# Performance work log

Measured on AMD Instinct MI355X. Metric: run time of the kernel, lower is better.

Reference implementation:

```python
import jax, jax.numpy as jnp
import numpy as np

# node types: 0=atac_region 1=gene 2=tad 3=protein 4=protein_name 5=enhancer
N = [25000, 15000, 4000, 12000, 12000, 15000]
FEAT = [257, 129, 128, 128, 129, 128]
# 19 relations of the HeteroConv, as (src_type, dst_type)
REL = [(2,0),(0,2),(2,1),(1,2),(0,1),(1,0),(3,3),(3,1),(1,3),(3,1),(1,3),(3,4),(4,3),(5,0),(0,5),(5,1),(1,5),(0,1),(1,0)]
E = 100000
H, HID = 128, 256
NAMES = ['atac','gene','tad','protein','pname','enh']


def setup_inputs():
    rng = np.random.default_rng(0)
    w = lambda *s: jnp.asarray((rng.standard_normal(s) / np.sqrt(s[-2])).astype(np.float32))
    z = lambda *s: jnp.zeros(s, dtype=jnp.float32)
    inp = {}
    for L in (0, 1):
        for t, nm in enumerate(NAMES):
            inp[f"x_{nm}{L}"] = jnp.asarray(rng.standard_normal((N[t], FEAT[t])).astype(np.float32))
            # sorted unique global node ids (x_map)
            inp[f"map_{nm}{L}"] = jnp.asarray(np.sort(rng.choice(2 * N[t], size=N[t], replace=False)).astype(np.int32))
        e = np.empty((len(REL), 2, E), dtype=np.int32)
        for r, (s, d) in enumerate(REL):
            e[r, 0] = rng.integers(0, N[s], E)
            e[r, 1] = rng.integers(0, N[d], E)
        inp[f"edges{L}"] = jnp.asarray(e)
    inp.update(W_in_atac=w(257, H), b_in_atac=z(H), W_in_gene=w(129, H), b_in_gene=z(H), W_in_pname=w(129, H), b_in_pname=z(H))
    inp.update(conv_wl=w(19, H, H), conv_bl=z(19, H), conv_wr=w(19, H, H))
    inp.update(mlp_w1=w(6, H, HID), mlp_b1=z(6, HID), mlp_w2=w(6, HID, H), mlp_b2=z(6, H))
    inp.update(gd_w1=w(H, HID), gd_b1=z(HID), gd_w2=w(HID, 1), gd_b2=z(1),
               gv_w1=w(H, HID), gv_b1=z(HID), gv_w2=w(HID, 1), gv_b2=z(1))
    return inp


def _sage(x_src, x_dst, eidx, wl, bl, wr):
    # PyG SAGEConv: out = lin_l(mean_{j in N(i)} x_src[j]) + lin_r(x_dst[i])
    src, dst = eidx[0], eidx[1]
    nd = x_dst.shape[0]
    agg = jax.ops.segment_sum(x_src[src], dst, num_segments=nd)
    cnt = jax.ops.segment_sum(jnp.ones((src.shape[0],), x_src.dtype), dst, num_segments=nd)
    mean = agg / jnp.maximum(cnt, 1.0)[:, None]
    return mean @ wl + bl + x_dst @ wr


def _hetero(xs, edges, wl, bl, wr):
    # HeteroConv with default sum aggregation across relations sharing a dst type
    out = {}
    for r, (s, d) in enumerate(REL):
        o = _sage(xs[s], xs[d], edges[r], wl[r], bl[r], wr[r])
        out[d] = out[d] + o if d in out else o
    return out


def _forward(fl, maps0, maps1, edges0, edges1):
    (x_atac0, x_gene0, x_tad0, x_protein0, x_pname0, x_enh0,
     x_atac1, x_gene1, x_tad1, x_protein1, x_pname1, x_enh1,
     W_in_atac, b_in_atac, W_in_gene, b_in_gene, W_in_pname, b_in_pname,
     conv_wl, conv_bl, conv_wr,
     mlp_w1, mlp_b1, mlp_w2, mlp_b2,
     gd_w1, gd_b1, gd_w2, gd_b2, gv_w1, gv_b1, gv_w2, gv_b2) = fl
    # input_linear applied to protein_name / atac_region / gene of every layer snapshot
    xs0 = [x_atac0 @ W_in_atac + b_in_atac, x_gene0 @ W_in_gene + b_in_gene, x_tad0,
           x_protein0, x_pname0 @ W_in_pname + b_in_pname, x_enh0]
    xs1 = [x_atac1 @ W_in_atac + b_in_atac, x_gene1 @ W_in_gene + b_in_gene, x_tad1,
           x_protein1, x_pname1 @ W_in_pname + b_in_pname, x_enh1]
    # layer 0 hetero conv + per-node-type layer MLP
    new0 = _hetero(xs0, edges0, conv_wl, conv_bl, conv_wr)
    new0 = {d: jax.nn.relu(x @ mlp_w1[d] + mlp_b1[d]) @ mlp_w2[d] + mlp_b2[d] for d, x in new0.items()}
    # mask-based cross-layer scatter: next_layer.x[dst_mask] = new_x[src_mask]
    # (x_maps sorted & unique -> equivalent gather via argmax of the O(N^2) equality mask)
    for d, x in new0.items():
        Mm = maps0[d][:, None] == maps1[d][None, :]   # [N0_d, N1_d] bool
        dst_mask = Mm.any(axis=0)                      # next-layer nodes present in layer 0
        pos = jnp.argmax(Mm, axis=0)                   # matching layer-0 row per next node
        xs1[d] = jnp.where(dst_mask[:, None], x[pos], xs1[d])
    # final layer: hetero conv only (no layer MLP, per encode())
    new1 = _hetero(xs1, edges1, conv_wl, conv_bl, conv_wr)
    g = new1[1]  # target = 'gene'
    p_drop = jax.nn.sigmoid(jax.nn.relu(g @ gd_w1 + gd_b1) @ gd_w2 + gd_b2)
    values = jax.nn.relu(g @ gv_w1 + gv_b1) @ gv_w2 + gv_b2
    return jnp.concatenate([p_drop, values], axis=-1)  # [N_gene, 2]


def reference(x_atac0, x_gene0, x_tad0, x_protein0, x_pname0, x_enh0,
              x_atac1, x_gene1, x_tad1, x_protein1, x_pname1, x_enh1,
              map_atac0, map_gene0, map_tad0, map_protein0, map_pname0, map_enh0,
              map_atac1, map_gene1, map_tad1, map_protein1, map_pname1, map_enh1,
              edges0, edges1,
              W_in_atac, b_in_atac, W_in_gene, b_in_gene, W_in_pname, b_in_pname,
              conv_wl, conv_bl, conv_wr,
              mlp_w1, mlp_b1, mlp_w2, mlp_b2,
              gd_w1, gd_b1, gd_w2, gd_b2, gv_w1, gv_b1, gv_w2, gv_b2):
    maps0 = [map_atac0, map_gene0, map_tad0, map_protein0, map_pname0, map_enh0]
    maps1 = [map_atac1, map_gene1, map_tad1, map_protein1, map_pname1, map_enh1]
    fl = (x_atac0, x_gene0, x_tad0, x_protein0, x_pname0, x_enh0,
          x_atac1, x_gene1, x_tad1, x_protein1, x_pname1, x_enh1,
          W_in_atac, b_in_atac, W_in_gene, b_in_gene, W_in_pname, b_in_pname,
          conv_wl, conv_bl, conv_wr,
          mlp_w1, mlp_b1, mlp_w2, mlp_b2,
          gd_w1, gd_b1, gd_w2, gd_b2, gv_w1, gv_b1, gv_w2, gv_b2)
    return _forward(fl, maps0, maps1, edges0, edges1)
```

## Files before the change

### kernel.cpp

```cpp
#include <hip/hip_runtime.h>
#include <math.h>

#define E_EDGES 100000

typedef unsigned short u16;
typedef unsigned int u32;

using bfrag = __attribute__((ext_vector_type(8))) short;
using ffrag = __attribute__((ext_vector_type(4))) float;

__device__ inline float bf2f(u32 u) { union { u32 i; float f; } c; c.i = u << 16; return c.f; }
__device__ inline u16 f2bf(float f) {
  union { u32 i; float f; } c; c.f = f;
  u32 u = c.i;
  return (u16)((u + 0x7FFFu + ((u >> 16) & 1u)) >> 16);
}

struct CsrArgs { int relid[24]; int lay[24]; int nd[24]; int rpoff[24];
                 int bkoff[24]; int bboff[24]; int nb[24]; };

struct AggAllArgs {
  const u16* xsrc[18];
  const int* rowptr[18];
  const int* esrc[18];
  u16* dst[18];
  int nd[18]; int pitch[18]; int koff[18];
};

struct WTStackArgs {
  int srcrel[23]; int grp[23]; long outoff[23]; int koff[23]; int pitch[23];
  int gnr[5]; int grel[5][6];
};

struct WTArgs { const float* W[15]; u16* out[15]; int K[15]; int N[15]; int Kpad[15]; };
struct PadArgs { const float* src[11]; u16* dst[11]; int K[11]; int Kpad8[11];
                 int total[11]; int aligned[11]; };
struct InLinBArgs { const u16* A[5]; const u16* WT[5]; const float* bias[5]; u16* C[5];
                    int M[5]; int Kpad[5]; };
struct FusedArgs {
  const u16* A[5]; const u16* selfA[5]; const u16* WTC[5]; const float* biasC[5];
  const u16* W1[5]; const float* b1[5]; const u16* W2[5]; const float* b2[5];
  const int* POS[5]; u16* C[5]; int M[5]; int kself[5]; int Kpad[5];
};
struct PosArgs { const int* m0[5]; const int* m1[5]; int* pos[5]; int n[5]; };
struct HeadArgs { const u16* WT[2]; const float* b1[2]; float* hid[2]; const u16* A; int M; };
struct HeadRArgs { const float* hid[2]; const float* w2[2]; const float* b2[2]; float* out; int M; };

__global__ __launch_bounds__(256) void tgemm_inb(InLinBArgs a)
{
  const int z = blockIdx.z;
  const int M = a.M[z], Kpad = a.Kpad[z];
  const int rowbase = blockIdx.x * 64;
  if (rowbase >= M) return;
  __shared__ u16 sA[64 * 40];
  __shared__ u16 sB[128 * 40];
  const int tid = threadIdx.x;
  const int w = tid >> 6, lane = tid & 63;
  const int quad = lane >> 4, m = lane & 15;
  const int sr = tid >> 2, sc = tid & 3;
  const int br = tid >> 1, bh = tid & 1;
  const u16* A = a.A[z];
  const u16* WT = a.WT[z];
  ffrag acc[8];
  #pragma unroll
  for (int i = 0; i < 8; i++) { acc[i][0] = 0.f; acc[i][1] = 0.f; acc[i][2] = 0.f; acc[i][3] = 0.f; }

  for (int kt = 0; kt < Kpad / 32; kt++) {
    int gr = rowbase + sr, gk = kt * 32 + sc * 8;
    uint4 st = make_uint4(0, 0, 0, 0);
    if (gr < M) st = *(const uint4*)(A + (long)gr * Kpad + gk);
    const u16* wrow = WT + (long)br * Kpad + kt * 32 + bh * 16;
    uint4 b0 = *(const uint4*)wrow;
    uint4 b1 = *(const uint4*)(wrow + 8);

    if (kt) __syncthreads();
    *(uint4*)&sA[sr * 40 + sc * 8] = st;
    *(uint4*)&sB[br * 40 + bh * 16] = b0;
    *(uint4*)&sB[br * 40 + bh * 16 + 8] = b1;
    __syncthreads();

    bfrag av = *(const bfrag*)&sA[(w * 16 + m) * 40 + quad * 8];
    #pragma unroll
    for (int ct = 0; ct < 8; ct++) {
      bfrag bv = *(const bfrag*)&sB[(ct * 16 + m) * 40 + quad * 8];
      acc[ct] = __builtin_amdgcn_mfma_f32_16x16x32_bf16(av, bv, acc[ct], 0, 0, 0);
    }
  }

  const float* bias = a.bias[z];
  u16* C = a.C[z];
  #pragma unroll
  for (int ct = 0; ct < 8; ct++) {
    int col = ct * 16 + m;
    float bv = bias[col];
    #pragma unroll
    for (int r = 0; r < 4; r++) {
      int row = rowbase + w * 16 + quad * 4 + r;
      if (row < M) C[(long)row * 128 + col] = f2bf(acc[ct][r] + bv);
    }
  }
}

__global__ __launch_bounds__(256) void fused_mlp(FusedArgs a)
{
  const int z = blockIdx.z;
  const int M = a.M[z];
  const int rowbase = blockIdx.x * 64;
  if (rowbase >= M) return;
  __shared__ u16 LDS[25088];
  u16* sB  = LDS;
  u16* sA  = LDS + 5120;
  u16* m1  = LDS + 7680;
  u16* m2b = LDS + 5120;
  u16* m2a = LDS + 16384;
  const int tid = threadIdx.x;
  const int w = tid >> 6, lane = tid & 63;
  const int quad = lane >> 4, m = lane & 15;
  const int sr = tid >> 2, sc = tid & 3;
  const int br = tid >> 1, bh = tid & 1;
  const int kself = a.kself[z], Kpad = a.Kpad[z];
  const u16* A = a.A[z];
  const u16* selfA = a.selfA[z];

  {
    const u16* WT = a.WTC[z];
    ffrag acc[8];
    #pragma unroll
    for (int i = 0; i < 8; i++) { acc[i][0] = 0.f; acc[i][1] = 0.f; acc[i][2] = 0.f; acc[i][3] = 0.f; }
    for (int kt = 0; kt < Kpad / 32; kt++) {
      int gr = rowbase + sr, gk = kt * 32 + sc * 8;
      uint4 st = make_uint4(0, 0, 0, 0);
      if (gr < M) {
        const u16* src = (gk < kself) ? (A + (long)gr * kself + gk)
                                      : (selfA + (long)gr * 128 + (gk - kself));
        st = *(const uint4*)src;
      }
      const u16* wrow = WT + (long)br * Kpad + kt * 32 + bh * 16;
      uint4 b0 = *(const uint4*)wrow;
      uint4 b1 = *(const uint4*)(wrow + 8);

      if (kt) __syncthreads();
      *(uint4*)&sA[sr * 40 + sc * 8] = st;
      *(uint4*)&sB[br * 40 + bh * 16] = b0;
      *(uint4*)&sB[br * 40 + bh * 16 + 8] = b1;
      __syncthreads();

      bfrag av = *(const bfrag*)&sA[(w * 16 + m) * 40 + quad * 8];
      #pragma unroll
      for (int ct = 0; ct < 8; ct++) {
        bfrag bv = *(const bfrag*)&sB[(ct * 16 + m) * 40 + quad * 8];
        acc[ct] = __builtin_amdgcn_mfma_f32_16x16x32_bf16(av, bv, acc[ct], 0, 0, 0);
      }
    }
    const float* bc = a.biasC[z];
    #pragma unroll
    for (int ct = 0; ct < 8; ct++) {
      int col = ct * 16 + m;
      float bv = bc[col];
      #pragma unroll
      for (int r = 0; r < 4; r++) {
        int row = w * 16 + quad * 4 + r;
        m1[row * 136 + col] = f2bf(acc[ct][r] + bv);
      }
    }
  }

  {
    const u16* W1 = a.W1[z];
    const float* b1p = a.b1[z];
    for (int h = 0; h < 2; h++) {
      ffrag acch[8];
      #pragma unroll
      for (int i = 0; i < 8; i++) { acch[i][0] = 0.f; acch[i][1] = 0.f; acch[i][2] = 0.f; acch[i][3] = 0.f; }
      for (int kt = 0; kt < 4; kt++) {
        const u16* wrow = W1 + (long)(h * 128 + br) * 128 + kt * 32 + bh * 16;
        uint4 b0 = *(const uint4*)wrow;
        uint4 b1v = *(const uint4*)(wrow + 8);
        __syncthreads();
        *(uint4*)&sB[br * 40 + bh * 16] = b0;
        *(uint4*)&sB[br * 40 + bh * 16 + 8] = b1v;
        __syncthreads();
        bfrag av = *(const bfrag*)&m1[(w * 16 + m) * 136 + kt * 32 + quad * 8];
        #pragma unroll
        for (int ct = 0; ct < 8; ct++) {
          bfrag bv = *(const bfrag*)&sB[(ct * 16 + m) * 40 + quad * 8];
          acch[ct] = __builtin_amdgcn_mfma_f32_16x16x32_bf16(av, bv, acch[ct], 0, 0, 0);
        }
      }
      u16* dstm = h ? m2b : m2a;
      if (h) __syncthreads();
      #pragma unroll
      for (int ct = 0; ct < 8; ct++) {
        int col = ct * 16 + m;
        float bv = b1p[h * 128 + col];
        #pragma unroll
        for (int r = 0; r < 4; r++) {
          int row = w * 16 + quad * 4 + r;
          dstm[row * 136 + col] = f2bf(fmaxf(acch[ct][r] + bv, 0.f));
        }
      }
    }
  }

  {
    const u16* W2 = a.W2[z];
    ffrag acc2[8];
    #pragma unroll
    for (int i = 0; i < 8; i++) { acc2[i][0] = 0.f; acc2[i][1] = 0.f; acc2[i][2] = 0.f; acc2[i][3] = 0.f; }
    for (int kt = 0; kt < 8; kt++) {
      const u16* wrow = W2 + (long)br * 256 + kt * 32 + bh * 16;
      uint4 b0 = *(const uint4*)wrow;
      uint4 b1v = *(const uint4*)(wrow + 8);
      __syncthreads();
      *(uint4*)&sB[br * 40 + bh * 16] = b0;
      *(uint4*)&sB[br * 40 + bh * 16 + 8] = b1v;
      __syncthreads();
      const u16* msrc = (kt < 4) ? m2a : m2b;
      bfrag av = *(const bfrag*)&msrc[(w * 16 + m) * 136 + (kt & 3) * 32 + quad * 8];
      #pragma unroll
      for (int ct = 0; ct < 8; ct++) {
        bfrag bv = *(const bfrag*)&sB[(ct * 16 + m) * 40 + quad * 8];
        acc2[ct] = __builtin_amdgcn_mfma_f32_16x16x32_bf16(av, bv, acc2[ct], 0, 0, 0);
      }
    }
    const int* POS = a.POS[z];
    const float* b2p = a.b2[z];
    u16* C = a.C[z];
    #pragma unroll
    for (int ct = 0; ct < 8; ct++) {
      int col = ct * 16 + m;
      float bv = b2p[col];
      #pragma unroll
      for (int r = 0; r < 4; r++) {
        int row = rowbase + w * 16 + quad * 4 + r;
        if (row < M) {
          int j = POS[row];
          if (j >= 0) C[(long)j * 128 + col] = f2bf(acc2[ct][r] + bv);
        }
      }
    }
  }
}

__global__ __launch_bounds__(256) void conv_l1(const u16* __restrict__ A,
                                               const u16* __restrict__ selfA,
                                               const u16* __restrict__ WT,
                                               const float* __restrict__ bias,
                                               u16* __restrict__ C,
                                               int M, int kself, int Kpad)
{
  const int rowbase = blockIdx.x * 64;
  if (rowbase >= M) return;
  __shared__ u16 sA[64 * 40];
  __shared__ u16 sB[128 * 40];
  const int tid = threadIdx.x;
  const int w = tid >> 6, lane = tid & 63;
  const int quad = lane >> 4, m = lane & 15;
  const int sr = tid >> 2, sc = tid & 3;
  const int br = tid >> 1, bh = tid & 1;
  ffrag acc[8];
  #pragma unroll
  for (int i = 0; i < 8; i++) { acc[i][0] = 0.f; acc[i][1] = 0.f; acc[i][2] = 0.f; acc[i][3] = 0.f; }

  for (int kt = 0; kt < Kpad / 32; kt++) {
    int gr = rowbase + sr, gk = kt * 32 + sc * 8;
    uint4 st = make_uint4(0, 0, 0, 0);
    if (gr < M) {
      const u16* src = (gk < kself) ? (A + (long)gr * kself + gk)
                                    : (selfA + (long)gr * 128 + (gk - kself));
      st = *(const uint4*)src;
    }
    const u16* wrow = WT + (long)br * Kpad + kt * 32 + bh * 16;
    uint4 b0 = *(const uint4*)wrow;
    uint4 b1 = *(const uint4*)(wrow + 8);

    if (kt) __syncthreads();
    *(uint4*)&sA[sr * 40 + sc * 8] = st;
    *(uint4*)&sB[br * 40 + bh * 16] = b0;
    *(uint4*)&sB[br * 40 + bh * 16 + 8] = b1;
    __syncthreads();

    bfrag av = *(const bfrag*)&sA[(w * 16 + m) * 40 + quad * 8];
    #pragma unroll
    for (int ct = 0; ct < 8; ct++) {
      bfrag bv = *(const bfrag*)&sB[(ct * 16 + m) * 40 + quad * 8];
      acc[ct] = __builtin_amdgcn_mfma_f32_16x16x32_bf16(av, bv, acc[ct], 0, 0, 0);
    }
  }

  #pragma unroll
  for (int ct = 0; ct < 8; ct++) {
    int col = ct * 16 + m;
    float bv = bias[col];
    #pragma unroll
    for (int r = 0; r < 4; r++) {
      int row = rowbase + w * 16 + quad * 4 + r;
      if (row < M) C[(long)row * 128 + col] = f2bf(acc[ct][r] + bv);
    }
  }
}

__global__ __launch_bounds__(256) void padcvt_kernel(PadArgs a)
{
  const int z = blockIdx.y;
  int idx = blockIdx.x * 256 + threadIdx.x;
  if (idx >= a.total[z]) return;
  const int kp8 = a.Kpad8[z];
  const int K = a.K[z];
  int row = idx / kp8;
  int c8 = idx - row * kp8;
  int base = c8 * 8;
  u32 wv[4];
  if (a.aligned[z]) {
    const float4* src = (const float4*)(a.src[z] + (long)row * K + base);
    float4 f0 = src[0];
    float4 f1 = src[1];
    wv[0] = (u32)f2bf(f0.x) | ((u32)f2bf(f0.y) << 16);
    wv[1] = (u32)f2bf(f0.z) | ((u32)f2bf(f0.w) << 16);
    wv[2] = (u32)f2bf(f1.x) | ((u32)f2bf(f1.y) << 16);
    wv[3] = (u32)f2bf(f1.z) | ((u32)f2bf(f1.w) << 16);
  } else {
    const float* src = a.src[z] + (long)row * K + base;
    #pragma unroll
    for (int i = 0; i < 4; i++) {
      float lo = (base + 2 * i     < K) ? src[2 * i]     : 0.f;
      float hi = (base + 2 * i + 1 < K) ? src[2 * i + 1] : 0.f;
      wv[i] = (u32)f2bf(lo) | ((u32)f2bf(hi) << 16);
    }
  }
  *(uint4*)(a.dst[z] + (long)row * (kp8 * 8) + base) = make_uint4(wv[0], wv[1], wv[2], wv[3]);
}

__global__ __launch_bounds__(256) void tgemm_head(HeadArgs a)
{
  const int z = blockIdx.z;
  const int M = a.M;
  const int rowbase = blockIdx.x * 64;
  const int colbase = blockIdx.y * 128;
  __shared__ u16 sA[64 * 40];
  __shared__ u16 sB[128 * 40];
  const int tid = threadIdx.x;
  const int w = tid >> 6, lane = tid & 63;
  const int quad = lane >> 4, m = lane & 15;
  const int sr = tid >> 2, sc = tid & 3;
  const int br = tid >> 1, bh = tid & 1;
  const u16* A = a.A;
  const u16* WT = a.WT[z];
  ffrag acc[8];
  #pragma unroll
  for (int i = 0; i < 8; i++) { acc[i][0] = 0.f; acc[i][1] = 0.f; acc[i][2] = 0.f; acc[i][3] = 0.f; }

  for (int kt = 0; kt < 4; kt++) {
    int gr = rowbase + sr, gk = kt * 32 + sc * 8;
    uint4 st = make_uint4(0, 0, 0, 0);
    if (gr < M) st = *(const uint4*)(A + (long)gr * 128 + gk);
    const u16* wrow = WT + (long)(colbase + br) * 128 + kt * 32 + bh * 16;
    uint4 b0 = *(const uint4*)wrow;
    uint4 b1 = *(const uint4*)(wrow + 8);

    if (kt) __syncthreads();
    *(uint4*)&sA[sr * 40 + sc * 8] = st;
    *(uint4*)&sB[br * 40 + bh * 16] = b0;
    *(uint4*)&sB[br * 40 + bh * 16 + 8] = b1;
    __syncthreads();

    bfrag av = *(const bfrag*)&sA[(w * 16 + m) * 40 + quad * 8];
    #pragma unroll
    for (int ct = 0; ct < 8; ct++) {
      bfrag bv = *(const bfrag*)&sB[(ct * 16 + m) * 40 + quad * 8];
      acc[ct] = __builtin_amdgcn_mfma_f32_16x16x32_bf16(av, bv, acc[ct], 0, 0, 0);
    }
  }

  const float* bias = a.b1[z];
  float* C = a.hid[z];
  #pragma unroll
  for (int ct = 0; ct < 8; ct++) {
    int col = colbase + ct * 16 + m;
    float bv = bias[col];
    #pragma unroll
    for (int r = 0; r < 4; r++) {
      int row = rowbase + w * 16 + quad * 4 + r;
      if (row < M) C[(long)row * 256 + col] = fmaxf(acc[ct][r] + bv, 0.f);
    }
  }
}

__global__ __launch_bounds__(256) void bhist_kernel(const int* __restrict__ e0,
                                                    const int* __restrict__ e1,
                                                    int* __restrict__ bcnt, CsrArgs a)
{
  const int slot = blockIdx.x / 25;
  const int ch = blockIdx.x % 25;
  const int base = ch * 4096;
  const int n = (E_EDGES - base < 4096) ? (E_EDGES - base) : 4096;
  const int* E = a.lay[slot] ? e1 : e0;
  const int r = a.relid[slot];
  const int tid = threadIdx.x;
  __shared__ int h[256];
  h[tid] = 0;
  __syncthreads();
  const int* darr = E + (r * 2 + 1) * E_EDGES + base;
  for (int i = tid; i < n; i += 256) atomicAdd(&h[darr[i] >> 7], 1);
  __syncthreads();
  if (tid < a.nb[slot] && h[tid]) atomicAdd(&bcnt[a.bkoff[slot] + tid], h[tid]);
}

__global__ __launch_bounds__(256) void bscan_kernel(const int* __restrict__ bcnt,
                                                    int* __restrict__ bbase,
                                                    int* __restrict__ bcur, CsrArgs a)
{
  int slot = blockIdx.x;
  int nb = a.nb[slot];
  int tid = threadIdx.x, lane = tid & 63, w = tid >> 6;
  __shared__ int ws[4];
  int v = (tid < nb) ? bcnt[a.bkoff[slot] + tid] : 0;
  int si = v;
  #pragma unroll
  for (int off = 1; off < 64; off <<= 1) {
    int t = __shfl_up(si, off, 64);
    if (lane >= off) si += t;
  }
  if (lane == 63) ws[w] = si;
  __syncthreads();
  int woff = 0;
  #pragma unroll
  for (int k = 0; k < 4; k++) if (k < w) woff += ws[k];
  int excl = woff + si - v;
  if (tid < nb) { bbase[a.bboff[slot] + tid] = excl; bcur[a.bkoff[slot] + tid] = excl; }
  if (tid == 0) bbase[a.bboff[slot] + nb] = ws[0] + ws[1] + ws[2] + ws[3];
}

__global__ __launch_bounds__(256) void bucket_scatter(const int* __restrict__ e0,
                                                      const int* __restrict__ e1,
                                                      int* __restrict__ bcur,
                                                      u32* __restrict__ tmp, CsrArgs a)
{
  const int slot = blockIdx.x / 25;
  const int ch = blockIdx.x % 25;
  const int base = ch * 4096;
  const int n = (E_EDGES - base < 4096) ? (E_EDGES - base) : 4096;
  const int* E = a.lay[slot] ? e1 : e0;
  const int r = a.relid[slot];
  const int nb = a.nb[slot];
  const int tid = threadIdx.x;
  __shared__ int hist[256], start[256], gbase[256], lcur[256];
  __shared__ u32 sorted[4096];
  hist[tid] = 0;
  __syncthreads();
  const int* darr = E + (r * 2 + 1) * E_EDGES + base;
  const int* sarr = E + r * 2 * E_EDGES + base;
  for (int i = tid; i < n; i += 256) atomicAdd(&hist[darr[i] >> 7], 1);
  __syncthreads();
  if (tid == 0) {
    int s = 0;
    for (int b = 0; b < nb; b++) { start[b] = s; s += hist[b]; }
  }
  __syncthreads();
  if (tid < nb) {
    gbase[tid] = atomicAdd(&bcur[a.bkoff[slot] + tid], hist[tid]);
    lcur[tid] = start[tid];
  }
  __syncthreads();
  for (int i = tid; i < n; i += 256) {
    int dst = darr[i], src = sarr[i];
    int pos = atomicAdd(&lcur[dst >> 7], 1);
    sorted[pos] = ((u32)dst << 16) | (u32)src;
  }
  __syncthreads();
  u32* out = tmp + (long)slot * E_EDGES;
  for (int i = tid; i < n; i += 256) {
    u32 p = sorted[i];
    int b = p >> 23;
    out[gbase[b] + (i - start[b])] = p;
  }
}

__global__ __launch_bounds__(256) void bucket_to_csr(const u32* __restrict__ tmp,
                                                     const int* __restrict__ bbase,
                                                     int* __restrict__ rp,
                                                     int* __restrict__ esrc, CsrArgs a)
{
  const int b = blockIdx.x, slot = blockIdx.y;
  if (b >= a.nb[slot]) return;
  const int rb = a.rpoff[slot];
  const int bb = bbase[a.bboff[slot] + b];
  const int be = bbase[a.bboff[slot] + b + 1];
  const int cnt = be - bb;
  const int rowlo = b << 7;
  int rowhi = rowlo + 128; if (rowhi > a.nd[slot]) rowhi = a.nd[slot];
  const int nrow = rowhi - rowlo;
  const int tid = threadIdx.x;
  __shared__ int rcnt[128];
  __shared__ int rpref[129];
  __shared__ int scur[128];
  __shared__ u32 sbuf[8192];
  if (tid < 128) rcnt[tid] = 0;
  __syncthreads();
  const u32* in = tmp + (long)slot * E_EDGES + bb;
  for (int i = tid; i < cnt; i += 256) atomicAdd(&rcnt[(in[i] >> 16) & 127], 1);
  __syncthreads();
  if (tid == 0) {
    int s = 0;
    for (int t = 0; t < 128; t++) { rpref[t] = s; s += rcnt[t]; }
    rpref[128] = s;
  }
  __syncthreads();
  if (tid < nrow) rp[rb + rowlo + tid] = bb + rpref[tid];
  if (tid == 0) rp[rb + rowhi] = be;
  if (tid < 128) scur[tid] = rpref[tid];
  __syncthreads();
  int* out = esrc + (long)slot * E_EDGES + bb;
  if (cnt <= 8192) {
    for (int i = tid; i < cnt; i += 256) {
      u32 p = in[i];
      int pos = atomicAdd(&scur[(p >> 16) & 127], 1);
      sbuf[pos] = p & 0xFFFFu;
    }
    __syncthreads();
    for (int i = tid; i < cnt; i += 256) out[i] = (int)sbuf[i];
  } else {
    for (int i = tid; i < cnt; i += 256) {
      u32 p = in[i];
      int pos = atomicAdd(&scur[(p >> 16) & 127], 1);
      out[pos] = (int)(p & 0xFFFFu);
    }
  }
}

__global__ __launch_bounds__(256) void wtstack_kernel(const float* __restrict__ wl,
                                                      const float* __restrict__ wr,
                                                      const float* __restrict__ bl,
                                                      u16* __restrict__ WTG,
                                                      float* __restrict__ BLS, WTStackArgs a)
{
  int slot = blockIdx.y;
  int t = blockIdx.x * 256 + threadIdx.x;
  int krel = t & 127, n = t >> 7;
  int sr = a.srcrel[slot];
  float v;
  if (sr >= 0) {
    v = wl[(long)sr * 16384 + krel * 128 + n];
  } else {
    int g = a.grp[slot];
    v = 0.f;
    for (int i = 0; i < a.gnr[g]; i++) v += wr[(long)a.grel[g][i] * 16384 + krel * 128 + n];
    if (t < 128) {
      float b = 0.f;
      for (int i = 0; i < a.gnr[g]; i++) b += bl[a.grel[g][i] * 128 + t];
      BLS[g * 128 + t] = b;
    }
  }
  WTG[a.outoff[slot] + (long)n * a.pitch[slot] + a.koff[slot] + krel] = f2bf(v);
}

__global__ __launch_bounds__(256) void wt_kernel(WTArgs a)
{
  int s = blockIdx.y;
  int idx = blockIdx.x * 256 + threadIdx.x;
  int K = a.K[s], N = a.N[s], Kpad = a.Kpad[s];
  if (idx >= N * Kpad) return;
  int n = idx / Kpad, k = idx - n * Kpad;
  a.out[s][idx] = (k < K) ? f2bf(a.W[s][(long)k * N + n]) : (u16)0;
}

__global__ __launch_bounds__(256) void pos_kernel(PosArgs a)
{
  int g = blockIdx.y;
  int i = blockIdx.x * 256 + threadIdx.x;
  if (i >= a.n[g]) return;
  int key = a.m0[g][i];
  const int* m1 = a.m1[g];
  int lo = 0, hi = a.n[g] - 1, pos = -1;
  while (lo <= hi) {
    int mid = (lo + hi) >> 1;
    int v = m1[mid];
    if (v == key) { pos = mid; break; }
    if (v < key) lo = mid + 1; else hi = mid - 1;
  }
  a.pos[g][i] = pos;
}

__global__ __launch_bounds__(256) void agg_all(AggAllArgs a)
{
  int slot = blockIdx.y;
  int grp = threadIdx.x >> 4;
  int lane = threadIdx.x & 15;
  int row = blockIdx.x * 16 + grp;
  if (row >= a.nd[slot]) return;
  u16* dst = a.dst[slot] + (long)row * a.pitch[slot] + a.koff[slot] + lane * 8;
  const uint4* x4 = (const uint4*)a.xsrc[slot];
  const int* rp = a.rowptr[slot];
  int c0 = rp[row], c1 = rp[row + 1];
  const int* es = a.esrc[slot];
  float acc[8];
  #pragma unroll
  for (int i = 0; i < 8; i++) acc[i] = 0.f;
  int e = c0;
  for (; e + 4 <= c1; e += 4) {
    int s0 = es[e], s1 = es[e + 1], s2 = es[e + 2], s3 = es[e + 3];
    uint4 v0 = x4[(long)s0 * 16 + lane];
    uint4 v1 = x4[(long)s1 * 16 + lane];
    uint4 v2 = x4[(long)s2 * 16 + lane];
    uint4 v3 = x4[(long)s3 * 16 + lane];
    const u32* w0 = (const u32*)&v0;
    const u32* w1 = (const u32*)&v1;
    const u32* w2 = (const u32*)&v2;
    const u32* w3 = (const u32*)&v3;
    #pragma unroll
    for (int i = 0; i < 4; i++) {
      acc[2*i]   += bf2f(w0[i] & 0xFFFF) + bf2f(w1[i] & 0xFFFF)
                  + bf2f(w2[i] & 0xFFFF) + bf2f(w3[i] & 0xFFFF);
      acc[2*i+1] += bf2f(w0[i] >> 16) + bf2f(w1[i] >> 16)
                  + bf2f(w2[i] >> 16) + bf2f(w3[i] >> 16);
    }
  }
  for (; e < c1; e++) {
    uint4 v = x4[(long)es[e] * 16 + lane];
    const u32* wv = (const u32*)&v;
    #pragma unroll
    for (int i = 0; i < 4; i++) {
      acc[2*i]   += bf2f(wv[i] & 0xFFFF);
      acc[2*i+1] += bf2f(wv[i] >> 16);
    }
  }
  int c = c1 - c0;
  float inv = 1.f / (float)(c > 1 ? c : 1);
  u32 o[4];
  #pragma unroll
  for (int i = 0; i < 4; i++)
    o[i] = (u32)f2bf(acc[2*i] * inv) | ((u32)f2bf(acc[2*i+1] * inv) << 16);
  *(uint4*)dst = make_uint4(o[0], o[1], o[2], o[3]);
}

__global__ __launch_bounds__(256) void head_reduce2(HeadRArgs a)
{
  int wave = threadIdx.x >> 6, lane = threadIdx.x & 63;
  int row = blockIdx.x * 4 + wave;
  int z = blockIdx.y;
  if (row >= a.M) return;
  const float* h = a.hid[z] + (long)row * 256;
  const float* w2 = a.w2[z];
  float s = h[lane] * w2[lane] + h[lane + 64] * w2[lane + 64]
          + h[lane + 128] * w2[lane + 128] + h[lane + 192] * w2[lane + 192];
  #pragma unroll
  for (int off = 32; off >= 1; off >>= 1) s += __shfl_down(s, off, 64);
  if (lane == 0) {
    float v = s + a.b2[z][0];
    if (z == 0) v = 1.0f / (1.0f + expf(-v));
    a.out[row * 2 + z] = v;
  }
}

extern "C" void kernel_launch(void* const* d_in, const int* in_sizes, int n_in,
                              void* d_out, int out_size, void* d_ws, size_t ws_size,
                              hipStream_t stream)
{
  static const int NT[6] = {25000, 15000, 4000, 12000, 12000, 15000};
  static const int REL_S[19] = {2,0,2,1,0,1,3,3,1,3,1,3,4,5,0,5,1,0,1};
  static const int REL_D[19] = {0,2,1,2,1,0,3,1,3,1,3,4,3,0,5,1,5,1,0};

  auto xin   = [&](int t, int L) { return (const float*)d_in[L * 13 + 2 * t]; };
  auto mapin = [&](int t, int L) { return (const int*)d_in[L * 13 + 2 * t + 1]; };
  const int* edges0 = (const int*)d_in[12];
  const int* edges1 = (const int*)d_in[25];
  const float* W_in_atac  = (const float*)d_in[26];
  const float* b_in_atac  = (const float*)d_in[27];
  const float* W_in_gene  = (const float*)d_in[28];
  const float* b_in_gene  = (const float*)d_in[29];
  const float* W_in_pname = (const float*)d_in[30];
  const float* b_in_pname = (const float*)d_in[31];
  const float* conv_wl = (const float*)d_in[32];
  const float* conv_bl = (const float*)d_in[33];
  const float* conv_wr = (const float*)d_in[34];
  const float* mlp_w1 = (const float*)d_in[35];
  const float* mlp_b1 = (const float*)d_in[36];
  const float* mlp_w2 = (const float*)d_in[37];
  const float* mlp_b2 = (const float*)d_in[38];
  const float* gd_w1 = (const float*)d_in[39];
  const float* gd_b1 = (const float*)d_in[40];
  const float* gd_w2 = (const float*)d_in[41];
  const float* gd_b2 = (const float*)d_in[42];
  const float* gv_w1 = (const float*)d_in[43];
  const float* gv_b1 = (const float*)d_in[44];
  const float* gv_w2 = (const float*)d_in[45];
  const float* gv_b2 = (const float*)d_in[46];
  float* out = (float*)d_out;

  static const int GD[5]       = {0, 1, 2, 3, 5};
  static const int GNR[5]      = {4, 6, 2, 4, 2};
  static const int GRELS[5][6] = {{0,5,13,18,0,0},{2,4,7,9,15,17},{1,3,0,0,0,0},
                                  {6,8,10,12,0,0},{14,16,0,0,0,0}};
  static const int GPITCH[5]   = {640, 896, 384, 640, 384};
  static const int GPA[5]      = {512, 768, 256, 512, 256};

  float* fp = (float*)d_ws;
  auto takef = [&](size_t n) { float* q = fp; fp += n; return q; };
  float* BLS  = takef(5 * 128);
  u16* bp = (u16*)fp;
  auto takeb = [&](size_t n) { u16* q = bp; bp += n; return q; };
  u16* XB0[6]; u16* XB1[6];
  XB0[0] = takeb((size_t)25000 * 128);
  XB0[1] = takeb((size_t)15000 * 128);
  XB0[2] = takeb((size_t)4000 * 128);
  XB0[3] = takeb((size_t)12000 * 128);
  XB0[4] = takeb((size_t)12000 * 128);
  XB0[5] = takeb((size_t)15000 * 128);
  XB1[0] = takeb((size_t)25000 * 128);
  XB1[1] = takeb((size_t)15000 * 128);
  XB1[2] = takeb((size_t)4000 * 128);
  XB1[3] = takeb((size_t)12000 * 128);
  XB1[4] = nullptr;
  XB1[5] = takeb((size_t)15000 * 128);
  u16* ABUF = takeb((size_t)35328000);
  u16* ABUFg[5];
  {
    long o = 0;
    for (int g = 0; g < 5; g++) { ABUFg[g] = ABUF + o; o += (long)NT[GD[g]] * GPA[g]; }
  }
  u16* G1B  = takeb((size_t)15000 * 128);
  u16* WTG  = takeb(376832);
  u16* WTIA = takeb(128 * 288);
  u16* WTIG = takeb(128 * 160);
  u16* WTIP = takeb(128 * 160);
  u16* WTM1 = takeb((size_t)5 * 32768);
  u16* WTM2 = takeb((size_t)5 * 32768);
  u16* WTHD = takeb(32768);
  u16* WTHV = takeb(32768);
  uintptr_t ipa = ((uintptr_t)bp + 15) & ~(uintptr_t)15;
  int* ip = (int*)ipa;
  auto takei = [&](size_t n) { int* q = ip; ip += n; return q; };
  int* RP    = takei(366024);
  int* BCNT  = takei(4704);
  int* BBASE = takei(4728);
  int* BCUR  = takei(4704);
  int* POSB  = takei(71000);
  int* ESRC  = takei((size_t)24 * E_EDGES);
  u32* TMP = (u32*)ABUF;
  float* HIDF0 = (float*)ABUF;
  float* HIDF1 = (float*)(ABUF + (size_t)15000 * 256 * 2);
  u16* PAD[5];
  PAD[0] = ABUF;
  PAD[1] = ABUF +  7200000;
  PAD[2] = ABUF +  9600000;
  PAD[3] = ABUF + 11520000;
  PAD[4] = ABUF + 18720000;

  long gbaseT[5];
  {
    long o = 0;
    for (int g = 0; g < 5; g++) { gbaseT[g] = o; o += (long)128 * GPITCH[g]; }
  }
  int* POSg[5];
  {
    int o = 0;
    for (int g = 0; g < 5; g++) { POSg[g] = POSB + o; o += NT[GD[g]]; }
  }

  {
    WTStackArgs wa{};
    int j = 0;
    for (int g = 0; g < 5; g++) {
      wa.gnr[g] = GNR[g];
      for (int i = 0; i < 6; i++) wa.grel[g][i] = GRELS[g][i];
      for (int s = 0; s <= GNR[g]; s++, j++) {
        wa.srcrel[j] = (s < GNR[g]) ? GRELS[g][s] : -1;
        wa.grp[j] = g;
        wa.outoff[j] = gbaseT[g];
        wa.koff[j] = s * 128;
        wa.pitch[j] = GPITCH[g];
      }
    }
    hipLaunchKernelGGL(wtstack_kernel, dim3(64, 23), dim3(256), 0, stream,
                       conv_wl, conv_wr, conv_bl, WTG, BLS, wa);
  }
  {
    WTArgs pa{};
    int s = 0;
    auto add = [&](const float* W, u16* o, int K, int N, int Kpad) {
      pa.W[s] = W; pa.out[s] = o; pa.K[s] = K; pa.N[s] = N; pa.Kpad[s] = Kpad; s++;
    };
    add(W_in_atac,  WTIA, 257, 128, 288);
    add(W_in_gene,  WTIG, 129, 128, 160);
    add(W_in_pname, WTIP, 129, 128, 160);
    for (int g = 0; g < 5; g++) {
      int d = GD[g];
      add(mlp_w1 + (long)d * 128 * 256, WTM1 + (long)g * 32768, 128, 256, 128);
      add(mlp_w2 + (long)d * 256 * 128, WTM2 + (long)g * 32768, 256, 128, 256);
    }
    add(gd_w1, WTHD, 128, 256, 128);
    add(gv_w1, WTHV, 128, 256, 128);
    hipLaunchKernelGGL(wt_kernel, dim3(144, 15), dim3(256), 0, stream, pa);
  }
  {
    PosArgs pa{};
    for (int g = 0; g < 5; g++) {
      int d = GD[g];
      pa.m0[g] = mapin(d, 0); pa.m1[g] = mapin(d, 1); pa.pos[g] = POSg[g]; pa.n[g] = NT[d];
    }
    hipLaunchKernelGGL(pos_kernel, dim3(98, 5), dim3(256), 0, stream, pa);
  }

  {
    PadArgs pc{};
    auto addp = [&](int s, const float* src, u16* dst, int M, int K, int Kpad) {
      pc.src[s] = src; pc.dst[s] = dst; pc.K[s] = K;
      pc.Kpad8[s] = Kpad / 8; pc.total[s] = M * (Kpad / 8);
      pc.aligned[s] = ((K & 7) == 0) ? 1 : 0;
    };
    addp(0, xin(0,0), PAD[0], 25000, 257, 288);
    addp(1, xin(1,0), PAD[1], 15000, 129, 160);
    addp(2, xin(4,0), PAD[2], 12000, 129, 160);
    addp(3, xin(0,1), PAD[3], 25000, 257, 288);
    addp(4, xin(1,1), PAD[4], 15000, 129, 160);
    addp(5, xin(2,0), XB0[2],  4000, 128, 128);
    addp(6, xin(3,0), XB0[3], 12000, 128, 128);
    addp(7, xin(5,0), XB0[5], 15000, 128, 128);
    addp(8, xin(2,1), XB1[2],  4000, 128, 128);
    addp(9, xin(3,1), XB1[3], 12000, 128, 128);
    addp(10, xin(5,1), XB1[5], 15000, 128, 128);
    hipLaunchKernelGGL(padcvt_kernel, dim3(3516, 11), dim3(256), 0, stream, pc);

    InLinBArgs ia{};
    auto add = [&](int s, const u16* A, const u16* WT, const float* b, u16* C,
                   int M, int Kpad) {
      ia.A[s] = A; ia.WT[s] = WT; ia.bias[s] = b; ia.C[s] = C;
      ia.M[s] = M; ia.Kpad[s] = Kpad;
    };
    add(0, PAD[0], WTIA, b_in_atac,  XB0[0], 25000, 288);
    add(1, PAD[1], WTIG, b_in_gene,  XB0[1], 15000, 160);
    add(2, PAD[2], WTIP, b_in_pname, XB0[4], 12000, 160);
    add(3, PAD[3], WTIA, b_in_atac,  XB1[0], 25000, 288);
    add(4, PAD[4], WTIG, b_in_gene,  XB1[1], 15000, 160);
    hipLaunchKernelGGL(tgemm_inb, dim3(391, 1, 5), dim3(256), 0, stream, ia);
  }

  static const int L0R[18] = {0,1,2,3,4,5,6,7,8,9,10,12,13,14,15,16,17,18};
  static const int L1R[6]  = {2, 4, 7, 9, 15, 17};
  int rpoffByRel[19], slotByRel[19], rpoff1[19], slot1[19];
  CsrArgs cc{};
  {
    int ro = 0, bo = 0, s = 0;
    for (int i = 0; i < 18; i++, s++) {
      int r = L0R[i];
      cc.relid[s] = r; cc.lay[s] = 0; int nd = NT[REL_D[r]];
      cc.nd[s] = nd; cc.rpoff[s] = ro;
      cc.bkoff[s] = bo; cc.bboff[s] = bo + s; cc.nb[s] = (nd + 127) >> 7;
      rpoffByRel[r] = ro; slotByRel[r] = s;
      ro += nd + 1; bo += cc.nb[s];
    }
    for (int i = 0; i < 6; i++, s++) {
      int r = L1R[i];
      cc.relid[s] = r; cc.lay[s] = 1;
      cc.nd[s] = 15000; cc.rpoff[s] = ro;
      cc.bkoff[s] = bo; cc.bboff[s] = bo + s; cc.nb[s] = (15000 + 127) >> 7;
      rpoff1[r] = ro; slot1[r] = s;
      ro += 15001; bo += cc.nb[s];
    }
    hipMemsetAsync(BCNT, 0, (size_t)bo * 4, stream);
    hipLaunchKernelGGL(bhist_kernel, dim3(24 * 25), dim3(256), 0, stream, edges0, edges1, BCNT, cc);
    hipLaunchKernelGGL(bscan_kernel, dim3(24), dim3(256), 0, stream, BCNT, BBASE, BCUR, cc);
    hipLaunchKernelGGL(bucket_scatter, dim3(24 * 25), dim3(256), 0, stream,
                       edges0, edges1, BCUR, TMP, cc);
    hipLaunchKernelGGL(bucket_to_csr, dim3(196, 24), dim3(256), 0, stream, TMP, BBASE, RP, ESRC, cc);
  }

  {
    AggAllArgs aa{};
    int j = 0;
    for (int g = 0; g < 5; g++) {
      int d = GD[g];
      for (int i = 0; i < GNR[g]; i++, j++) {
        int r = GRELS[g][i];
        aa.xsrc[j]   = XB0[REL_S[r]];
        aa.rowptr[j] = RP + rpoffByRel[r];
        aa.esrc[j]   = ESRC + (long)slotByRel[r] * E_EDGES;
        aa.dst[j] = ABUFg[g]; aa.nd[j] = NT[d]; aa.pitch[j] = GPA[g];
        aa.koff[j] = i * 128;
      }
    }
    hipLaunchKernelGGL(agg_all, dim3(1563, 18), dim3(256), 0, stream, aa);
  }
  {
    FusedArgs fa{};
    for (int g = 0; g < 5; g++) {
      int d = GD[g];
      fa.A[g] = ABUFg[g]; fa.selfA[g] = XB0[d];
      fa.WTC[g] = WTG + gbaseT[g]; fa.biasC[g] = BLS + g * 128;
      fa.W1[g] = WTM1 + (long)g * 32768; fa.b1[g] = mlp_b1 + d * 256;
      fa.W2[g] = WTM2 + (long)g * 32768; fa.b2[g] = mlp_b2 + d * 128;
      fa.POS[g] = POSg[g]; fa.C[g] = XB1[d];
      fa.M[g] = NT[d]; fa.kself[g] = GPA[g]; fa.Kpad[g] = GPITCH[g];
    }
    hipLaunchKernelGGL(fused_mlp, dim3(391, 1, 5), dim3(256), 0, stream, fa);
  }

  {
    AggAllArgs aa{};
    for (int i = 0; i < 6; i++) {
      int r = L1R[i];
      aa.xsrc[i]   = XB1[REL_S[r]];
      aa.rowptr[i] = RP + rpoff1[r];
      aa.esrc[i]   = ESRC + (long)slot1[r] * E_EDGES;
      aa.dst[i] = ABUF; aa.nd[i] = 15000; aa.pitch[i] = 768;
      aa.koff[i] = i * 128;
    }
    hipLaunchKernelGGL(agg_all, dim3(938, 6), dim3(256), 0, stream, aa);
    hipLaunchKernelGGL(conv_l1, dim3(235), dim3(256), 0, stream,
                       ABUF, XB1[1], WTG + gbaseT[1], BLS + 1 * 128, G1B,
                       15000, 768, 896);
  }

  {
    HeadArgs ha{};
    ha.WT[0] = WTHD; ha.WT[1] = WTHV;
    ha.b1[0] = gd_b1; ha.b1[1] = gv_b1;
    ha.hid[0] = HIDF0; ha.hid[1] = HIDF1;
    ha.A = G1B; ha.M = 15000;
    hipLaunchKernelGGL(tgemm_head, dim3(235, 2, 2), dim3(256), 0, stream, ha);
    HeadRArgs hr{};
    hr.hid[0] = HIDF0; hr.hid[1] = HIDF1;
    hr.w2[0] = gd_w2; hr.w2[1] = gv_w2;
    hr.b2[0] = gd_b2; hr.b2[1] = gv_b2;
    hr.out = out; hr.M = 15000;
    hipLaunchKernelGGL(head_reduce2, dim3(3750, 2), dim3(256), 0, stream, hr);
  }
}
```

Baseline: 519.0 us.

## Load MLP weight and input fragments directly from global, interleave second GEMM per half

The fused MLP kernel stops staging A and weight tiles through LDS with barriers each k-step. Each wave now reads its MFMA operands straight from global memory, relying on the cache for weight reuse across waves. The hidden layer is produced in two 128-column halves, and each half is multiplied by the second-layer weights right away. This drops one LDS buffer and many syncs, and the LDS stride changes to 152. In exchange, every wave issues redundant uncoalesced global loads for the weights, which may cost more memory latency.

```diff
diff --git a/kernel.cpp b/kernel.cpp
--- a/kernel.cpp
+++ b/kernel.cpp
@@ -101,26 +101,24 @@
   }
 }
 
+#define MSTR 152
 __global__ __launch_bounds__(256) void fused_mlp(FusedArgs a)
 {
   const int z = blockIdx.z;
   const int M = a.M[z];
   const int rowbase = blockIdx.x * 64;
   if (rowbase >= M) return;
-  __shared__ u16 LDS[25088];
-  u16* sB  = LDS;
-  u16* sA  = LDS + 5120;
-  u16* m1  = LDS + 7680;
-  u16* m2b = LDS + 5120;
-  u16* m2a = LDS + 16384;
+  __shared__ u16 LDS[2 * 64 * MSTR];
+  u16* m1 = LDS;
+  u16* m2 = LDS + 64 * MSTR;
   const int tid = threadIdx.x;
   const int w = tid >> 6, lane = tid & 63;
   const int quad = lane >> 4, m = lane & 15;
-  const int sr = tid >> 2, sc = tid & 3;
-  const int br = tid >> 1, bh = tid & 1;
   const int kself = a.kself[z], Kpad = a.Kpad[z];
   const u16* A = a.A[z];
   const u16* selfA = a.selfA[z];
+  const int arow = rowbase + w * 16 + m;
+  const int orow = w * 16 + quad * 4;
 
   {
     const u16* WT = a.WTC[z];
@@ -128,27 +126,18 @@
     #pragma unroll
     for (int i = 0; i < 8; i++) { acc[i][0] = 0.f; acc[i][1] = 0.f; acc[i][2] = 0.f; acc[i][3] = 0.f; }
     for (int kt = 0; kt < Kpad / 32; kt++) {
-      int gr = rowbase + sr, gk = kt * 32 + sc * 8;
-      uint4 st = make_uint4(0, 0, 0, 0);
-      if (gr < M) {
-        const u16* src = (gk < kself) ? (A + (long)gr * kself + gk)
-                                      : (selfA + (long)gr * 128 + (gk - kself));
-        st = *(const uint4*)src;
+      int gk = kt * 32 + quad * 8;
+      bfrag av;
+      if (arow < M) {
+        const u16* src = (gk < kself) ? (A + (long)arow * kself + gk)
+                                      : (selfA + (long)arow * 128 + (gk - kself));
+        av = *(const bfrag*)src;
+      } else {
+        av = bfrag{0,0,0,0,0,0,0,0};
       }
-      const u16* wrow = WT + (long)br * Kpad + kt * 32 + bh * 16;
-      uint4 b0 = *(const uint4*)wrow;
-      uint4 b1 = *(const uint4*)(wrow + 8);
-
-      if (kt) __syncthreads();
-      *(uint4*)&sA[sr * 40 + sc * 8] = st;
-      *(uint4*)&sB[br * 40 + bh * 16] = b0;
-      *(uint4*)&sB[br * 40 + bh * 16 + 8] = b1;
-      __syncthreads();
-
-      bfrag av = *(const bfrag*)&sA[(w * 16 + m) * 40 + quad * 8];
       #pragma unroll
       for (int ct = 0; ct < 8; ct++) {
-        bfrag bv = *(const bfrag*)&sB[(ct * 16 + m) * 40 + quad * 8];
+        bfrag bv = *(const bfrag*)(WT + (long)(ct * 16 + m) * Kpad + gk);
         acc[ct] = __builtin_amdgcn_mfma_f32_16x16x32_bf16(av, bv, acc[ct], 0, 0, 0);
       }
     }
@@ -158,71 +147,53 @@
       int col = ct * 16 + m;
       float bv = bc[col];
       #pragma unroll
-      for (int r = 0; r < 4; r++) {
-        int row = w * 16 + quad * 4 + r;
-        m1[row * 136 + col] = f2bf(acc[ct][r] + bv);
-      }
-    }
-  }
-
+      for (int r = 0; r < 4; r++)
+        m1[(orow + r) * MSTR + col] = f2bf(acc[ct][r] + bv);
+    }
+  }
+  __syncthreads();
+
+  ffrag acc2[8];
+  #pragma unroll
+  for (int i = 0; i < 8; i++) { acc2[i][0] = 0.f; acc2[i][1] = 0.f; acc2[i][2] = 0.f; acc2[i][3] = 0.f; }
   {
     const u16* W1 = a.W1[z];
+    const u16* W2 = a.W2[z];
     const float* b1p = a.b1[z];
     for (int h = 0; h < 2; h++) {
       ffrag acch[8];
       #pragma unroll
       for (int i = 0; i < 8; i++) { acch[i][0] = 0.f; acch[i][1] = 0.f; acch[i][2] = 0.f; acch[i][3] = 0.f; }
       for (int kt = 0; kt < 4; kt++) {
-        const u16* wrow = W1 + (long)(h * 128 + br) * 128 + kt * 32 + bh * 16;
-        uint4 b0 = *(const uint4*)wrow;
-        uint4 b1v = *(const uint4*)(wrow + 8);
-        __syncthreads();
-        *(uint4*)&sB[br * 40 + bh * 16] = b0;
-        *(uint4*)&sB[br * 40 + bh * 16 + 8] = b1v;
-        __syncthreads();
-        bfrag av = *(const bfrag*)&m1[(w * 16 + m) * 136 + kt * 32 + quad * 8];
+        bfrag av = *(const bfrag*)&m1[(w * 16 + m) * MSTR + kt * 32 + quad * 8];
         #pragma unroll
         for (int ct = 0; ct < 8; ct++) {
-          bfrag bv = *(const bfrag*)&sB[(ct * 16 + m) * 40 + quad * 8];
+          bfrag bv = *(const bfrag*)(W1 + (long)(h * 128 + ct * 16 + m) * 128 + kt * 32 + quad * 8);
           acch[ct] = __builtin_amdgcn_mfma_f32_16x16x32_bf16(av, bv, acch[ct], 0, 0, 0);
         }
       }
-      u16* dstm = h ? m2b : m2a;
       if (h) __syncthreads();
       #pragma unroll
       for (int ct = 0; ct < 8; ct++) {
         int col = ct * 16 + m;
         float bv = b1p[h * 128 + col];
         #pragma unroll
-        for (int r = 0; r < 4; r++) {
-          int row = w * 16 + quad * 4 + r;
-          dstm[row * 136 + col] = f2bf(fmaxf(acch[ct][r] + bv, 0.f));
+        for (int r = 0; r < 4; r++)
+          m2[(orow + r) * MSTR + col] = f2bf(fmaxf(acch[ct][r] + bv, 0.f));
+      }
+      __syncthreads();
+      for (int kt2 = 0; kt2 < 4; kt2++) {
+        bfrag av = *(const bfrag*)&m2[(w * 16 + m) * MSTR + kt2 * 32 + quad * 8];
+        #pragma unroll
+        for (int ct = 0; ct < 8; ct++) {
+          bfrag bv = *(const bfrag*)(W2 + (long)(ct * 16 + m) * 256 + h * 128 + kt2 * 32 + quad * 8);
+          acc2[ct] = __builtin_amdgcn_mfma_f32_16x16x32_bf16(av, bv, acc2[ct], 0, 0, 0);
         }
       }
     }
   }
 
   {
-    const u16* W2 = a.W2[z];
-    ffrag acc2[8];
-    #pragma unroll
-    for (int i = 0; i < 8; i++) { acc2[i][0] = 0.f; acc2[i][1] = 0.f; acc2[i][2] = 0.f; acc2[i][3] = 0.f; }
-    for (int kt = 0; kt < 8; kt++) {
-      const u16* wrow = W2 + (long)br * 256 + kt * 32 + bh * 16;
-      uint4 b0 = *(const uint4*)wrow;
-      uint4 b1v = *(const uint4*)(wrow + 8);
-      __syncthreads();
-      *(uint4*)&sB[br * 40 + bh * 16] = b0;
-      *(uint4*)&sB[br * 40 + bh * 16 + 8] = b1v;
-      __syncthreads();
-      const u16* msrc = (kt < 4) ? m2a : m2b;
-      bfrag av = *(const bfrag*)&msrc[(w * 16 + m) * 136 + (kt & 3) * 32 + quad * 8];
-      #pragma unroll
-      for (int ct = 0; ct < 8; ct++) {
-        bfrag bv = *(const bfrag*)&sB[(ct * 16 + m) * 40 + quad * 8];
-        acc2[ct] = __builtin_amdgcn_mfma_f32_16x16x32_bf16(av, bv, acc2[ct], 0, 0, 0);
-      }
-    }
     const int* POS = a.POS[z];
     const float* b2p = a.b2[z];
     u16* C = a.C[z];
@@ -232,7 +203,7 @@
       float bv = b2p[col];
       #pragma unroll
       for (int r = 0; r < 4; r++) {
-        int row = rowbase + w * 16 + quad * 4 + r;
+        int row = rowbase + orow + r;
         if (row < M) {
           int j = POS[row];
           if (j >= 0) C[(long)j * 128 + col] = f2bf(acc2[ct][r] + bv);
```

Result: slower. 664.9 us (+28.1%).
